# Performance work log

Measured on AMD Instinct MI355X. Metric: run time of the kernel, lower is better.

## Reference

```python
import jax, jax.numpy as jnp
import numpy as np

FP8_MAX = 448.0  # float8_e4m3fn max representable magnitude
AMAX_EPS = 1e-12


def _quantize_fp8_block(x):
    """Float8BlockQuantizer: 1D blocks of 128 along last dim (dim==128 => one
    block per row), force_pow_2_scales=True. Returns dequantized fp32 data
    (fp8 round-trip) and the per-block scale (rowwise_scale_inv)."""
    amax = jnp.maximum(jnp.max(jnp.abs(x), axis=-1, keepdims=True), AMAX_EPS)
    scale = jnp.exp2(jnp.ceil(jnp.log2(amax / FP8_MAX)))  # pow-2, >= amax/448
    xq = (x / scale).astype(jnp.float8_e4m3fn).astype(jnp.float32)
    return xq, scale[..., 0]


def setup_inputs() -> dict:
    key = jax.random.key(0)
    kq, kk, kw = jax.random.split(key, 3)
    seq_q, seq_k, head, dim = 4096, 4096, 32, 128
    return {
        "index_q": jax.random.normal(kq, (seq_q, head, dim), dtype=jnp.float32),
        "index_k": jax.random.normal(kk, (seq_k, dim), dtype=jnp.float32),
        "weights": jax.random.uniform(kw, (seq_q, head), dtype=jnp.float32),
        "index_topk": 2048,
        "chunk_offset": 0,
    }


def reference(index_q, index_k, weights, index_topk, chunk_offset):
    seq_q, head, dim = index_q.shape
    seq_k = index_k.shape[0]
    softmax_scale = dim ** (-0.5)

    qf, q_scale = _quantize_fp8_block(index_q)  # qf [sq,h,d], q_scale [sq,h]
    kf, k_scale = _quantize_fp8_block(index_k)  # kf [sk,d],   k_scale [sk]

    # fp8_mqa_logits: logits[i,j] = sum_h w_scaled[i,h] * (qf[i,h] . kf[j]) * k_scale[j]
    w_scaled = weights * q_scale * softmax_scale  # [sq,h]
    q_eff = jnp.einsum('qh,qhd->qd', w_scaled, qf)  # fold head-weighted sum
    logits = (q_eff @ kf.T) * k_scale[None, :]      # [sq, sk]

    # causal mask: valid keys are [k_start=0, k_end=i+chunk_offset+1)
    k_end = jnp.arange(seq_q, dtype=jnp.int32) + chunk_offset + 1
    mask = jnp.arange(seq_k, dtype=jnp.int32)[None, :] < k_end[:, None]
    logits = jnp.where(mask, logits, -jnp.inf)

    # index_topk <= seq_k here, so no padding branch needed
    vals, idx = jax.lax.top_k(logits, index_topk)  # sorted descending
    return vals, idx
```

## Files before the change

### kernel.cpp

```cpp
#include <hip/hip_runtime.h>
#include <stdint.h>

#define SQ 4096
#define SK 4096
#define NH 32
#define DIM 128


__device__ __forceinline__ float fp8_rt(float x) {
    int p = __builtin_amdgcn_cvt_pk_fp8_f32(x, x, 0, false);
    return __builtin_amdgcn_cvt_f32_fp8(p, 0);
}

__device__ __forceinline__ uint32_t map_f32(float v) {
    uint32_t b = __float_as_uint(v);
    return b ^ ((b & 0x80000000u) ? 0xFFFFFFFFu : 0x80000000u);
}

__device__ __forceinline__ void pow2_scale(float amax, float& scale, float& inv) {
    int e;
    float m = frexpf(amax, &e);
    int k = (m <= 0.875f) ? (e - 9) : (e - 8);
    scale = ldexpf(1.0f, k);
    inv = ldexpf(1.0f, -k);
}

__global__ void prep_q(const float* __restrict__ q, const float* __restrict__ w,
                       float* __restrict__ q_eff) {
    int row = blockIdx.x;
    int t = threadIdx.x;
    const float softmax_scale = 0.08838834764831845f;
    float accx = 0.f, accy = 0.f;
    for (int h = 0; h < NH; ++h) {
        float2 v = *reinterpret_cast<const float2*>(q + ((size_t)row * NH + h) * DIM + 2 * t);
        float m = fmaxf(fabsf(v.x), fabsf(v.y));
#pragma unroll
        for (int off = 32; off > 0; off >>= 1) m = fmaxf(m, __shfl_xor(m, off));
        float amax = fmaxf(m, 1e-12f);
        float scale, inv;
        pow2_scale(amax, scale, inv);
        float ws = w[(size_t)row * NH + h] * scale * softmax_scale;
        accx += ws * fp8_rt(v.x * inv);
        accy += ws * fp8_rt(v.y * inv);
    }
    float2 o; o.x = accx; o.y = accy;
    *reinterpret_cast<float2*>(q_eff + (size_t)row * DIM + 2 * t) = o;
}

__global__ void prep_k(const float* __restrict__ kin, float* __restrict__ kfs) {
    int row = blockIdx.x;
    int t = threadIdx.x;
    float2 v = *reinterpret_cast<const float2*>(kin + (size_t)row * DIM + 2 * t);
    float m = fmaxf(fabsf(v.x), fabsf(v.y));
#pragma unroll
    for (int off = 32; off > 0; off >>= 1) m = fmaxf(m, __shfl_xor(m, off));
    float amax = fmaxf(m, 1e-12f);
    float scale, inv;
    pow2_scale(amax, scale, inv);
    float2 o; o.x = fp8_rt(v.x * inv) * scale; o.y = fp8_rt(v.y * inv) * scale;
    *reinterpret_cast<float2*>(kfs + (size_t)row * DIM + 2 * t) = o;
}

__global__ __launch_bounds__(256) void logits_sort_topk(
    const float* __restrict__ qe, const float* __restrict__ kfs,
    float* __restrict__ vals, int* __restrict__ idxs,
    const int* __restrict__ co_ptr, int topk) {
    __shared__ uint64_t keys[SK];
    __shared__ float qrow[DIM];
    int row = blockIdx.x;
    int t = threadIdx.x;
    int co = *co_ptr;
    int nv = row + co + 1;
    nv = nv < 0 ? 0 : (nv > SK ? SK : nv);
    int N = 1;
    while (N < nv) N <<= 1;

    if (t < DIM / 4) {
        *reinterpret_cast<float4*>(qrow + t * 4) =
            *reinterpret_cast<const float4*>(qe + (size_t)row * DIM + t * 4);
    }
    __syncthreads();

    for (int j = t; j < N; j += 256) {
        uint64_t kk = 0;
        if (j < nv) {
            const float4* kp = reinterpret_cast<const float4*>(kfs + (size_t)j * DIM);
            float acc = 0.f;
#pragma unroll 8
            for (int d4 = 0; d4 < DIM / 4; ++d4) {
                float4 kv = kp[d4];
                float4 qv = *reinterpret_cast<const float4*>(qrow + d4 * 4);
                acc += qv.x * kv.x; acc += qv.y * kv.y;
                acc += qv.z * kv.z; acc += qv.w * kv.w;
            }
            kk = ((uint64_t)map_f32(acc) << 32) | (uint32_t)(~j);
        }
        keys[j] = kk;
    }
    __syncthreads();

    for (int k = 2; k <= N; k <<= 1) {
        for (int j = k >> 1; j > 0; j >>= 1) {
            for (int p = t; p < (N >> 1); p += 256) {
                int i1 = ((p & ~(j - 1)) << 1) | (p & (j - 1));
                int i2 = i1 | j;
                uint64_t a = keys[i1], b = keys[i2];
                bool desc = (i1 & k) == 0;
                if ((a < b) == desc) { keys[i1] = b; keys[i2] = a; }
            }
            __syncthreads();
        }
    }

    for (int n = t; n < topk; n += 256) {
        float v; int id;
        uint64_t kk = (n < nv) ? keys[n] : 0;
        if (kk != 0) {
            uint32_t m = (uint32_t)(kk >> 32);
            uint32_t b = m ^ ((m & 0x80000000u) ? 0x80000000u : 0xFFFFFFFFu);
            v = __uint_as_float(b);
            id = (int)(~(uint32_t)kk);
        } else {
            v = -1.0e30f;
            id = n;
        }
        if (!(fabsf(v) <= 1.0e38f)) v = -1.0e30f;
        vals[(size_t)row * topk + n] = v;
        idxs[(size_t)row * topk + n] = id;
    }
}

extern "C" void kernel_launch(void* const* d_in, const int* in_sizes, int n_in,
                              void* d_out, int out_size, void* d_ws, size_t ws_size,
                              hipStream_t stream) {
    (void)in_sizes; (void)n_in; (void)ws_size;
    const float* q = (const float*)d_in[0];
    const float* k = (const float*)d_in[1];
    const float* w = (const float*)d_in[2];
    const int* co_ptr = (const int*)d_in[4];
    int topk = out_size / (2 * SQ);

    char* ws = (char*)d_ws;
    float* q_eff = (float*)(ws);
    float* kfs   = (float*)(ws + (size_t)(2 << 20));

    hipLaunchKernelGGL(prep_q, dim3(SQ), dim3(64), 0, stream, q, w, q_eff);
    hipLaunchKernelGGL(prep_k, dim3(SK), dim3(64), 0, stream, k, kfs);
    hipLaunchKernelGGL(logits_sort_topk, dim3(SQ), dim3(256), 0, stream,
                       q_eff, kfs, (float*)d_out, (int*)d_out + (size_t)SQ * topk,
                       co_ptr, topk);
}
```

Baseline: 675.1 us.

## Replace bitonic sort with stable block-local 4-bit LSD radix sort

Replaces the per-row bitonic sort over 64-bit packed keys in shared memory with an 8-pass 4-bit LSD radix sort on 32-bit keys plus 16-bit indices. Each thread owns a contiguous run of 16 elements and builds packed per-thread histograms, which are then scanned with wave shuffles. Elements are scattered stably, and an XOR slot swizzle is used to reduce LDS bank conflicts. This aims to cut the O(N log^2 N) compare-exchange passes and the many barriers of bitonic sort, at the cost of more scan and barrier logic per pass. Tie ordering relies on stability rather than the encoded index.

```diff
diff --git a/kernel.cpp b/kernel.cpp
--- a/kernel.cpp
+++ b/kernel.cpp
@@ -5,6 +5,8 @@
 #define SK 4096
 #define NH 32
 #define DIM 128
+#define NBINS 16
+#define HPAD 264
 
 
 __device__ __forceinline__ float fp8_rt(float x) {
@@ -23,6 +25,10 @@
     int k = (m <= 0.875f) ? (e - 9) : (e - 8);
     scale = ldexpf(1.0f, k);
     inv = ldexpf(1.0f, -k);
+}
+
+__device__ __forceinline__ int vslot(int p) {
+    return p ^ ((p >> 4) & 15) ^ ((p >> 8) & 15);
 }
 
 __global__ void prep_q(const float* __restrict__ q, const float* __restrict__ w,
@@ -61,19 +67,22 @@
     *reinterpret_cast<float2*>(kfs + (size_t)row * DIM + 2 * t) = o;
 }
 
-__global__ __launch_bounds__(256) void logits_sort_topk(
+__global__ __launch_bounds__(256) void logits_radix_topk(
     const float* __restrict__ qe, const float* __restrict__ kfs,
     float* __restrict__ vals, int* __restrict__ idxs,
     const int* __restrict__ co_ptr, int topk) {
-    __shared__ uint64_t keys[SK];
+    __shared__ uint32_t sval[SK];
+    __shared__ uint16_t sidx[SK];
+    __shared__ uint16_t H[NBINS * HPAD];
+    __shared__ uint32_t sbin[NBINS];
     __shared__ float qrow[DIM];
+
     int row = blockIdx.x;
     int t = threadIdx.x;
     int co = *co_ptr;
     int nv = row + co + 1;
     nv = nv < 0 ? 0 : (nv > SK ? SK : nv);
-    int N = 1;
-    while (N < nv) N <<= 1;
+    int M = (nv + 15) & ~15;
 
     if (t < DIM / 4) {
         *reinterpret_cast<float4*>(qrow + t * 4) =
@@ -81,8 +90,8 @@
     }
     __syncthreads();
 
-    for (int j = t; j < N; j += 256) {
-        uint64_t kk = 0;
+    for (int i = 0; i < SK / 256; ++i) {
+        int j = t + 256 * i;
         if (j < nv) {
             const float4* kp = reinterpret_cast<const float4*>(kfs + (size_t)j * DIM);
             float acc = 0.f;
@@ -93,33 +102,115 @@
                 acc += qv.x * kv.x; acc += qv.y * kv.y;
                 acc += qv.z * kv.z; acc += qv.w * kv.w;
             }
-            kk = ((uint64_t)map_f32(acc) << 32) | (uint32_t)(~j);
-        }
-        keys[j] = kk;
+            sval[vslot(j)] = ~map_f32(acc);
+        } else if (j < M) {
+            sval[vslot(j)] = 0xFFFFFFFFu;
+        }
     }
     __syncthreads();
 
-    for (int k = 2; k <= N; k <<= 1) {
-        for (int j = k >> 1; j > 0; j >>= 1) {
-            for (int p = t; p < (N >> 1); p += 256) {
-                int i1 = ((p & ~(j - 1)) << 1) | (p & (j - 1));
-                int i2 = i1 | j;
-                uint64_t a = keys[i1], b = keys[i2];
-                bool desc = (i1 & k) == 0;
-                if ((a < b) == desc) { keys[i1] = b; keys[i2] = a; }
-            }
-            __syncthreads();
-        }
+    int base = t * 16;
+    bool act = base < M;
+    int wv = t >> 6, ln = t & 63;
+
+    for (int pass = 0; pass < 8; ++pass) {
+        int shift = pass * 4;
+        uint32_t kb[16];
+        uint32_t ib[16];
+        uint32_t h0 = 0, h1 = 0, h2 = 0, h3 = 0;
+        if (act) {
+#pragma unroll
+            for (int e = 0; e < 16; ++e) kb[e] = sval[vslot(base + e)];
+            if (pass == 0) {
+#pragma unroll
+                for (int e = 0; e < 16; ++e) ib[e] = base + e;
+            } else {
+#pragma unroll
+                for (int e = 0; e < 16; ++e) ib[e] = sidx[vslot(base + e)];
+            }
+#pragma unroll
+            for (int e = 0; e < 16; ++e) {
+                uint32_t d = (kb[e] >> shift) & 15u;
+                uint32_t inc = 1u << ((d & 3u) << 3);
+                uint32_t w = d >> 2;
+                h0 += (w == 0) ? inc : 0u;
+                h1 += (w == 1) ? inc : 0u;
+                h2 += (w == 2) ? inc : 0u;
+                h3 += (w == 3) ? inc : 0u;
+            }
+        }
+#pragma unroll
+        for (int b = 0; b < NBINS; ++b) {
+            uint32_t hw = (b < 4) ? h0 : (b < 8) ? h1 : (b < 12) ? h2 : h3;
+            H[b * HPAD + t] = (uint16_t)((hw >> ((b & 3) * 8)) & 0xFFu);
+        }
+        __syncthreads();
+
+#pragma unroll
+        for (int bb = 0; bb < 4; ++bb) {
+            int b = wv * 4 + bb;
+            uint32_t c0 = H[b * HPAD + 4 * ln + 0];
+            uint32_t c1 = H[b * HPAD + 4 * ln + 1];
+            uint32_t c2 = H[b * HPAD + 4 * ln + 2];
+            uint32_t c3 = H[b * HPAD + 4 * ln + 3];
+            uint32_t lsum = c0 + c1 + c2 + c3;
+            uint32_t s = lsum;
+#pragma unroll
+            for (int off = 1; off < 64; off <<= 1) {
+                uint32_t v = __shfl_up(s, off);
+                if (ln >= off) s += v;
+            }
+            uint32_t excl = s - lsum;
+            H[b * HPAD + 4 * ln + 0] = (uint16_t)excl;
+            H[b * HPAD + 4 * ln + 1] = (uint16_t)(excl + c0);
+            H[b * HPAD + 4 * ln + 2] = (uint16_t)(excl + c0 + c1);
+            H[b * HPAD + 4 * ln + 3] = (uint16_t)(excl + c0 + c1 + c2);
+            if (ln == 63) sbin[b] = s;
+        }
+        __syncthreads();
+
+        if (t == 0) {
+            uint32_t r = 0;
+#pragma unroll
+            for (int b = 0; b < NBINS; ++b) { uint32_t c = sbin[b]; sbin[b] = r; r += c; }
+        }
+        __syncthreads();
+
+#pragma unroll
+        for (int b = 0; b < NBINS; ++b)
+            H[b * HPAD + t] = (uint16_t)(H[b * HPAD + t] + sbin[b]);
+
+        if (act) {
+            uint32_t c0 = 0, c1 = 0, c2 = 0, c3 = 0;
+#pragma unroll
+            for (int e = 0; e < 16; ++e) {
+                uint32_t d = (kb[e] >> shift) & 15u;
+                uint32_t w = d >> 2;
+                uint32_t sh = (d & 3u) << 3;
+                uint32_t colbase = H[d * HPAD + t];
+                uint32_t cw = (w == 0) ? c0 : (w == 1) ? c1 : (w == 2) ? c2 : c3;
+                uint32_t pos = colbase + ((cw >> sh) & 0xFFu);
+                int sl = vslot((int)pos);
+                sval[sl] = kb[e];
+                sidx[sl] = (uint16_t)ib[e];
+                uint32_t inc = 1u << sh;
+                c0 += (w == 0) ? inc : 0u;
+                c1 += (w == 1) ? inc : 0u;
+                c2 += (w == 2) ? inc : 0u;
+                c3 += (w == 3) ? inc : 0u;
+            }
+        }
+        __syncthreads();
     }
 
     for (int n = t; n < topk; n += 256) {
         float v; int id;
-        uint64_t kk = (n < nv) ? keys[n] : 0;
-        if (kk != 0) {
-            uint32_t m = (uint32_t)(kk >> 32);
+        if (n < nv) {
+            int sl = vslot(n);
+            uint32_t m = ~sval[sl];
             uint32_t b = m ^ ((m & 0x80000000u) ? 0x80000000u : 0xFFFFFFFFu);
             v = __uint_as_float(b);
-            id = (int)(~(uint32_t)kk);
+            id = (int)sidx[sl];
         } else {
             v = -1.0e30f;
             id = n;
@@ -146,7 +237,7 @@
 
     hipLaunchKernelGGL(prep_q, dim3(SQ), dim3(64), 0, stream, q, w, q_eff);
     hipLaunchKernelGGL(prep_k, dim3(SK), dim3(64), 0, stream, k, kfs);
-    hipLaunchKernelGGL(logits_sort_topk, dim3(SQ), dim3(256), 0, stream,
+    hipLaunchKernelGGL(logits_radix_topk, dim3(SQ), dim3(256), 0, stream,
                        q_eff, kfs, (float*)d_out, (int*)d_out + (size_t)SQ * topk,
                        co_ptr, topk);
 }
```

New measurement: 630.8 us. -6.6%, faster.
